# Optimization experiments

Measured on AMD Instinct MI355X. Metric: run time of the kernel, lower is better.

## Reference

```python
import jax, jax.numpy as jnp
import numpy as np

N_TOTAL = 200000
DIM = 256
N_GRAPHS = 8192
N_ITERS = 6


def setup_inputs() -> dict:
    key = jax.random.key(0)
    k1, k2, k3, k4, k5, k6 = jax.random.split(key, 6)
    x = jax.random.normal(k1, (N_TOTAL, DIM), dtype=jnp.float32)
    batch = jnp.sort(jax.random.randint(k2, (N_TOTAL,), 0, N_GRAPHS)).astype(jnp.int32)
    bound = 1.0 / np.sqrt(DIM)
    W_ih = jax.random.uniform(k3, (4 * DIM, DIM), jnp.float32, -bound, bound)
    W_hh = jax.random.uniform(k4, (4 * DIM, DIM), jnp.float32, -bound, bound)
    b_ih = jax.random.uniform(k5, (4 * DIM,), jnp.float32, -bound, bound)
    b_hh = jax.random.uniform(k6, (4 * DIM,), jnp.float32, -bound, bound)
    return {"x": x, "batch": batch, "n_graphs": N_GRAPHS,
            "W_ih": W_ih, "W_hh": W_hh, "b_ih": b_ih, "b_hh": b_hh}


def _lstm_cell(inp, h, c, W_ih, W_hh, b_ih, b_hh):
    # PyTorch LSTMCell: gates ordered i, f, g, o
    gates = inp @ W_ih.T + b_ih + h @ W_hh.T + b_hh
    i, f, g, o = jnp.split(gates, 4, axis=-1)
    c_new = jax.nn.sigmoid(f) * c + jax.nn.sigmoid(i) * jnp.tanh(g)
    h_new = jax.nn.sigmoid(o) * jnp.tanh(c_new)
    return h_new, c_new


def reference(x, batch, n_graphs, W_ih, W_hh, b_ih, b_hh):
    dim = x.shape[1]
    h = jnp.zeros((n_graphs, dim), x.dtype)
    c = jnp.zeros((n_graphs, dim), x.dtype)
    readout = jnp.zeros((n_graphs, dim), x.dtype)
    for _ in range(N_ITERS):
        # attention scores per node: <x_v, q_{g(v)}>
        scores = jnp.sum(x * h[batch], axis=-1)  # (N,)
        # torch scatter_reduce_ amax with zero init includes the 0 -> max(seg_max, 0)
        seg_max = jax.ops.segment_max(scores, batch, num_segments=n_graphs,
                                      indices_are_sorted=True)
        seg_max = jnp.maximum(seg_max, 0.0)
        e = jnp.exp(scores - seg_max[batch])
        seg_sum = jax.ops.segment_sum(e, batch, num_segments=n_graphs,
                                      indices_are_sorted=True)
        w = e / (seg_sum[batch] + 1e-8)  # (N,)
        readout = jax.ops.segment_sum(x * w[:, None], batch, num_segments=n_graphs,
                                      indices_are_sorted=True)  # (G, dim)
        h, c = _lstm_cell(readout, h, c, W_ih, W_hh, b_ih, b_hh)
    return jnp.concatenate([h, readout], axis=-1)  # (G, 2*dim)
```

## Files before the change

### kernel.cpp

```cpp
#include <hip/hip_runtime.h>
#include <hip/hip_bf16.h>
#include <stdint.h>

#define DIM 256
#define NG 8192
#define KDIM 512
#define GDIM 1024
#define N_ITERS 6
#define CHUNK 32

#define BM 128
#define BN 128
#define BK 64

typedef __hip_bfloat16 bf16;
typedef __attribute__((ext_vector_type(8))) short bf16x8;
typedef __attribute__((ext_vector_type(4))) float f32x4;

__device__ __forceinline__ void async16(void* lds, const void* g) {
    __builtin_amdgcn_global_load_lds((const __attribute__((address_space(1))) void*)g,
                                     (__attribute__((address_space(3))) void*)lds, 16, 0, 0);
}

__device__ __forceinline__ float fast_sigmoid(float v) {
    return 1.0f / (1.0f + __expf(-v));
}
__device__ __forceinline__ float fast_tanh(float v) {
    float e = __expf(2.0f * v);
    return (e - 1.0f) / (e + 1.0f);
}

__global__ void k_offsets(const int* __restrict__ batch, int* __restrict__ offs, int n_nodes) {
    int v = blockIdx.x * blockDim.x + threadIdx.x;
    if (v >= n_nodes) return;
    int b = batch[v];
    int bp = (v == 0) ? -1 : batch[v - 1];
    for (int g = bp + 1; g <= b; ++g) offs[g] = v;
    if (v == n_nodes - 1) {
        for (int g = b + 1; g <= NG; ++g) offs[g] = n_nodes;
    }
}

__global__ void k_prep_w(const float* __restrict__ Wih, const float* __restrict__ Whh,
                         const float* __restrict__ bih, const float* __restrict__ bhh,
                         bf16* __restrict__ Wcat, float* __restrict__ bsum) {
    int idx = blockIdx.x * blockDim.x + threadIdx.x;
    if (idx < GDIM * KDIM) {
        int j = idx >> 9;
        int k = idx & (KDIM - 1);
        float v = (k < DIM) ? Wih[j * DIM + k] : Whh[j * DIM + (k - DIM)];
        Wcat[idx] = __float2bfloat16(v);
    }
    if (idx < GDIM) bsum[idx] = bih[idx] + bhh[idx];
}

__global__ void k_zero(float* __restrict__ h, float* __restrict__ c, bf16* __restrict__ Acat) {
    int i = blockIdx.x * blockDim.x + threadIdx.x;
    if (i < NG * DIM) { h[i] = 0.0f; c[i] = 0.0f; }
    if (i < NG * KDIM) Acat[i] = __float2bfloat16(0.0f);
}

__global__ __launch_bounds__(256) void k_att(const float* __restrict__ x,
                                             const float* __restrict__ h,
                                             const int* __restrict__ offs,
                                             float* __restrict__ readout,
                                             bf16* __restrict__ Acat) {
    const int g = blockIdx.x;
    const int tid = threadIdx.x;
    const int wave = tid >> 6, lane = tid & 63;

    __shared__ float xs[CHUNK][DIM];
    __shared__ float sc[CHUNK];
    __shared__ float esh[CHUNK];
    __shared__ float hs[DIM];

    hs[tid] = h[(size_t)g * DIM + tid];
    __syncthreads();
    const float4 hreg = *(const float4*)&hs[lane * 4];

    const int start = offs[g], end = offs[g + 1];
    float racc = 0.0f;
    float m = 0.0f;
    float s = 0.0f;

    for (int base = start; base < end; base += CHUNK) {
        const int cnt = min(CHUNK, end - base);
        for (int i = wave; i < cnt; i += 4) {
            const float4 xv = ((const float4*)(x + (size_t)(base + i) * DIM))[lane];
            ((float4*)xs[i])[lane] = xv;
            float d = xv.x * hreg.x + xv.y * hreg.y + xv.z * hreg.z + xv.w * hreg.w;
            #pragma unroll
            for (int off = 32; off > 0; off >>= 1) d += __shfl_xor(d, off);
            if (lane == 0) sc[i] = d;
        }
        __syncthreads();
        float cmax = m;
        for (int i = 0; i < cnt; ++i) cmax = fmaxf(cmax, sc[i]);
        const float alpha = __expf(m - cmax);
        racc *= alpha;
        s *= alpha;
        if (tid < cnt) esh[tid] = __expf(sc[tid] - cmax);
        m = cmax;
        __syncthreads();
        for (int i = 0; i < cnt; ++i) {
            const float e = esh[i];
            s += e;
            racc += e * xs[i][tid];
        }
        __syncthreads();
    }

    const float out = racc / (s + 1e-8f);
    readout[(size_t)g * DIM + tid] = out;
    Acat[(size_t)g * KDIM + tid] = __float2bfloat16(out);
}

__global__ __launch_bounds__(256) void k_gemm(const bf16* __restrict__ A,
                                              const bf16* __restrict__ B,
                                              const float* __restrict__ bsum,
                                              float* __restrict__ gates) {
    __shared__ bf16 As[BM * BK];
    __shared__ bf16 Bs[BN * BK];

    const int tid = threadIdx.x;
    const int wave = tid >> 6, lane = tid & 63;
    const int m0 = blockIdx.x * BM;
    const int n0 = blockIdx.y * BN;
    const int wr = wave >> 1, wc = wave & 1;

    f32x4 acc[4][4] = {};

    const int row_in_grp = lane >> 3;
    const int chunk = lane & 7;

    for (int k0 = 0; k0 < KDIM; k0 += BK) {
        #pragma unroll
        for (int i = 0; i < 4; ++i) {
            const int row = wave * 32 + i * 8 + row_in_grp;
            async16(&As[(wave * 32 + i * 8) * BK],
                    A + (size_t)(m0 + row) * KDIM + k0 + chunk * 8);
        }
        #pragma unroll
        for (int i = 0; i < 4; ++i) {
            const int row = wave * 32 + i * 8 + row_in_grp;
            async16(&Bs[(wave * 32 + i * 8) * BK],
                    B + (size_t)(n0 + row) * KDIM + k0 + chunk * 8);
        }
        asm volatile("s_waitcnt vmcnt(0)" ::: "memory");
        __syncthreads();

        #pragma unroll
        for (int ks = 0; ks < BK; ks += 32) {
            bf16x8 a[4], b[4];
            #pragma unroll
            for (int mi = 0; mi < 4; ++mi)
                a[mi] = *(const bf16x8*)&As[(wr * 64 + mi * 16 + (lane & 15)) * BK + ks + (lane >> 4) * 8];
            #pragma unroll
            for (int ni = 0; ni < 4; ++ni)
                b[ni] = *(const bf16x8*)&Bs[(wc * 64 + ni * 16 + (lane & 15)) * BK + ks + (lane >> 4) * 8];
            #pragma unroll
            for (int mi = 0; mi < 4; ++mi)
                #pragma unroll
                for (int ni = 0; ni < 4; ++ni)
                    acc[mi][ni] = __builtin_amdgcn_mfma_f32_16x16x32_bf16(a[mi], b[ni], acc[mi][ni], 0, 0, 0);
        }
        __syncthreads();
    }

    #pragma unroll
    for (int mi = 0; mi < 4; ++mi) {
        #pragma unroll
        for (int ni = 0; ni < 4; ++ni) {
            const int col = n0 + wc * 64 + ni * 16 + (lane & 15);
            const float bv = bsum[col];
            #pragma unroll
            for (int r = 0; r < 4; ++r) {
                const int row = m0 + wr * 64 + mi * 16 + (lane >> 4) * 4 + r;
                gates[(size_t)row * GDIM + col] = acc[mi][ni][r] + bv;
            }
        }
    }
}

__global__ void k_cell(const float* __restrict__ gates, float* __restrict__ c,
                       float* __restrict__ h, bf16* __restrict__ Acat) {
    int idx = blockIdx.x * blockDim.x + threadIdx.x;
    if (idx >= NG * DIM) return;
    const int g = idx >> 8, d = idx & (DIM - 1);
    const float* gr = gates + (size_t)g * GDIM;
    const float vi = gr[d];
    const float vf = gr[d + 256];
    const float vg = gr[d + 512];
    const float vo = gr[d + 768];
    const float cn = fast_sigmoid(vf) * c[idx] + fast_sigmoid(vi) * fast_tanh(vg);
    const float hn = fast_sigmoid(vo) * fast_tanh(cn);
    c[idx] = cn;
    h[idx] = hn;
    Acat[(size_t)g * KDIM + DIM + d] = __float2bfloat16(hn);
}

__global__ void k_out(const float* __restrict__ h, const float* __restrict__ readout,
                      float* __restrict__ out) {
    int idx = blockIdx.x * blockDim.x + threadIdx.x;
    if (idx >= NG * KDIM) return;
    const int g = idx >> 9, d = idx & (KDIM - 1);
    out[idx] = (d < DIM) ? h[(size_t)g * DIM + d] : readout[(size_t)g * DIM + (d - DIM)];
}

extern "C" void kernel_launch(void* const* d_in, const int* in_sizes, int n_in,
                              void* d_out, int out_size, void* d_ws, size_t ws_size,
                              hipStream_t stream) {
    const float* x     = (const float*)d_in[0];
    const int*   batch = (const int*)d_in[1];
    const float* Wih   = (const float*)d_in[3];
    const float* Whh   = (const float*)d_in[4];
    const float* bih   = (const float*)d_in[5];
    const float* bhh   = (const float*)d_in[6];
    const int n_nodes  = in_sizes[0] / DIM;
    float* out = (float*)d_out;

    char* ws = (char*)d_ws;
    size_t off = 0;
    auto alloc = [&](size_t bytes) -> void* {
        off = (off + 255) & ~(size_t)255;
        void* p = ws + off;
        off += bytes;
        return p;
    };
    int*   offs    = (int*)  alloc((size_t)(NG + 1) * sizeof(int));
    bf16*  Wcat    = (bf16*) alloc((size_t)GDIM * KDIM * sizeof(bf16));
    float* bsum    = (float*)alloc((size_t)GDIM * sizeof(float));
    bf16*  Acat    = (bf16*) alloc((size_t)NG * KDIM * sizeof(bf16));
    float* h       = (float*)alloc((size_t)NG * DIM * sizeof(float));
    float* c       = (float*)alloc((size_t)NG * DIM * sizeof(float));
    float* readout = (float*)alloc((size_t)NG * DIM * sizeof(float));
    float* gates   = (float*)alloc((size_t)NG * GDIM * sizeof(float));
    (void)ws_size; (void)n_in; (void)out_size;

    k_offsets<<<(n_nodes + 255) / 256, 256, 0, stream>>>(batch, offs, n_nodes);
    k_prep_w<<<(GDIM * KDIM + 255) / 256, 256, 0, stream>>>(Wih, Whh, bih, bhh, Wcat, bsum);
    k_zero<<<(NG * KDIM + 255) / 256, 256, 0, stream>>>(h, c, Acat);

    for (int it = 0; it < N_ITERS; ++it) {
        k_att<<<NG, 256, 0, stream>>>(x, h, offs, readout, Acat);
        k_gemm<<<dim3(NG / BM, GDIM / BN), 256, 0, stream>>>(Acat, Wcat, bsum, gates);
        k_cell<<<(NG * DIM + 255) / 256, 256, 0, stream>>>(gates, c, h, Acat);
    }
    k_out<<<(NG * KDIM + 255) / 256, 256, 0, stream>>>(h, readout, out);
}
```

Measured before the change: 838.5 us.

## Fuse LSTM cell into GEMM epilogue and cache x as fp16 after first pass

Interleaves the gate rows of the weight matrix so each GEMM tile holds all four gates for its hidden units, which lets the LSTM cell update run in the GEMM epilogue and removes the fp32 gates round trip and the separate cell kernel. The A operand is double-buffered so the fused epilogue can write the new h half without racing other tiles. The first attention pass also writes an fp16 copy of x, and later passes read that copy, halving the dominant x traffic. The risk is lower precision in the attention scores and readout from fp16 x, plus extra LDS syncs in the epilogue.

```diff
diff --git a/kernel.cpp b/kernel.cpp
--- a/kernel.cpp
+++ b/kernel.cpp
@@ -1,5 +1,6 @@
 #include <hip/hip_runtime.h>
 #include <hip/hip_bf16.h>
+#include <hip/hip_fp16.h>
 #include <stdint.h>
 
 #define DIM 256
@@ -16,18 +17,31 @@
 typedef __hip_bfloat16 bf16;
 typedef __attribute__((ext_vector_type(8))) short bf16x8;
 typedef __attribute__((ext_vector_type(4))) float f32x4;
+typedef __attribute__((ext_vector_type(8))) unsigned short u16x8;
+typedef __attribute__((ext_vector_type(4))) unsigned short u16x4;
 
 __device__ __forceinline__ void async16(void* lds, const void* g) {
     __builtin_amdgcn_global_load_lds((const __attribute__((address_space(1))) void*)g,
                                      (__attribute__((address_space(3))) void*)lds, 16, 0, 0);
 }
-
 __device__ __forceinline__ float fast_sigmoid(float v) {
     return 1.0f / (1.0f + __expf(-v));
 }
 __device__ __forceinline__ float fast_tanh(float v) {
     float e = __expf(2.0f * v);
     return (e - 1.0f) / (e + 1.0f);
+}
+__device__ __forceinline__ unsigned short f2bf(float v) {
+    __hip_bfloat16 t = __float2bfloat16(v);
+    unsigned short u; __builtin_memcpy(&u, &t, 2); return u;
+}
+__device__ __forceinline__ unsigned short f2h(float v) {
+    __half t = __float2half_rn(v);
+    unsigned short u; __builtin_memcpy(&u, &t, 2); return u;
+}
+__device__ __forceinline__ float h2f(unsigned short u) {
+    __half t; __builtin_memcpy(&t, &u, 2);
+    return __half2float(t);
 }
 
 __global__ void k_offsets(const int* __restrict__ batch, int* __restrict__ offs, int n_nodes) {
@@ -46,37 +60,50 @@
                          bf16* __restrict__ Wcat, float* __restrict__ bsum) {
     int idx = blockIdx.x * blockDim.x + threadIdx.x;
     if (idx < GDIM * KDIM) {
-        int j = idx >> 9;
+        int n = idx >> 9;
         int k = idx & (KDIM - 1);
+        int d = n >> 2, gate = n & 3;
+        int j = gate * DIM + d;
         float v = (k < DIM) ? Wih[j * DIM + k] : Whh[j * DIM + (k - DIM)];
         Wcat[idx] = __float2bfloat16(v);
     }
-    if (idx < GDIM) bsum[idx] = bih[idx] + bhh[idx];
-}
-
-__global__ void k_zero(float* __restrict__ h, float* __restrict__ c, bf16* __restrict__ Acat) {
+    if (idx < GDIM) {
+        int d = idx >> 2, gate = idx & 3;
+        int j = gate * DIM + d;
+        bsum[idx] = bih[j] + bhh[j];
+    }
+}
+
+__global__ void k_zero(float* __restrict__ h, float* __restrict__ c, bf16* __restrict__ Acat0) {
     int i = blockIdx.x * blockDim.x + threadIdx.x;
-    if (i < NG * DIM) { h[i] = 0.0f; c[i] = 0.0f; }
-    if (i < NG * KDIM) Acat[i] = __float2bfloat16(0.0f);
-}
-
-__global__ __launch_bounds__(256) void k_att(const float* __restrict__ x,
+    if (i >= NG * DIM) return;
+    h[i] = 0.0f; c[i] = 0.0f;
+    Acat0[(size_t)(i >> 8) * KDIM + DIM + (i & 255)] = __float2bfloat16(0.0f);
+}
+
+template <bool FIRST>
+__global__ __launch_bounds__(256) void k_att(const float* __restrict__ xf,
+                                             unsigned short* __restrict__ xb,
                                              const float* __restrict__ h,
                                              const int* __restrict__ offs,
                                              float* __restrict__ readout,
-                                             bf16* __restrict__ Acat) {
+                                             bf16* __restrict__ AcatOut) {
     const int g = blockIdx.x;
     const int tid = threadIdx.x;
     const int wave = tid >> 6, lane = tid & 63;
-
-    __shared__ float xs[CHUNK][DIM];
+    const int sub = lane >> 5, hl = lane & 31;
+
+    __shared__ unsigned short xs[CHUNK][DIM];
     __shared__ float sc[CHUNK];
     __shared__ float esh[CHUNK];
-    __shared__ float hs[DIM];
-
-    hs[tid] = h[(size_t)g * DIM + tid];
-    __syncthreads();
-    const float4 hreg = *(const float4*)&hs[lane * 4];
+
+    float hreg[8];
+    {
+        const float4 h0 = *(const float4*)&h[(size_t)g * DIM + hl * 8];
+        const float4 h1 = *(const float4*)&h[(size_t)g * DIM + hl * 8 + 4];
+        hreg[0] = h0.x; hreg[1] = h0.y; hreg[2] = h0.z; hreg[3] = h0.w;
+        hreg[4] = h1.x; hreg[5] = h1.y; hreg[6] = h1.z; hreg[7] = h1.w;
+    }
 
     const int start = offs[g], end = offs[g + 1];
     float racc = 0.0f;
@@ -85,13 +112,28 @@
 
     for (int base = start; base < end; base += CHUNK) {
         const int cnt = min(CHUNK, end - base);
-        for (int i = wave; i < cnt; i += 4) {
-            const float4 xv = ((const float4*)(x + (size_t)(base + i) * DIM))[lane];
-            ((float4*)xs[i])[lane] = xv;
-            float d = xv.x * hreg.x + xv.y * hreg.y + xv.z * hreg.z + xv.w * hreg.w;
-            #pragma unroll
-            for (int off = 32; off > 0; off >>= 1) d += __shfl_xor(d, off);
-            if (lane == 0) sc[i] = d;
+        for (int i = wave * 2; i < cnt; i += 8) {
+            const int r = i + sub;
+            if (r < cnt) {
+                u16x8 pk;
+                float dt = 0.0f;
+                if (FIRST) {
+                    const float4 a = *(const float4*)&xf[(size_t)(base + r) * DIM + hl * 8];
+                    const float4 b = *(const float4*)&xf[(size_t)(base + r) * DIM + hl * 8 + 4];
+                    float xv[8] = {a.x, a.y, a.z, a.w, b.x, b.y, b.z, b.w};
+                    #pragma unroll
+                    for (int j = 0; j < 8; ++j) { pk[j] = f2h(xv[j]); dt = fmaf(xv[j], hreg[j], dt); }
+                    *(u16x8*)&xb[(size_t)(base + r) * DIM + hl * 8] = pk;
+                } else {
+                    pk = *(const u16x8*)&xb[(size_t)(base + r) * DIM + hl * 8];
+                    #pragma unroll
+                    for (int j = 0; j < 8; ++j) dt = fmaf(h2f(pk[j]), hreg[j], dt);
+                }
+                *(u16x8*)&xs[r][hl * 8] = pk;
+                #pragma unroll
+                for (int off = 16; off > 0; off >>= 1) dt += __shfl_xor(dt, off);
+                if (hl == 0) sc[r] = dt;
+            }
         }
         __syncthreads();
         float cmax = m;
@@ -105,22 +147,26 @@
         for (int i = 0; i < cnt; ++i) {
             const float e = esh[i];
             s += e;
-            racc += e * xs[i][tid];
+            racc = fmaf(e, h2f(xs[i][tid]), racc);
         }
         __syncthreads();
     }
 
     const float out = racc / (s + 1e-8f);
     readout[(size_t)g * DIM + tid] = out;
-    Acat[(size_t)g * KDIM + tid] = __float2bfloat16(out);
-}
-
-__global__ __launch_bounds__(256) void k_gemm(const bf16* __restrict__ A,
-                                              const bf16* __restrict__ B,
-                                              const float* __restrict__ bsum,
-                                              float* __restrict__ gates) {
-    __shared__ bf16 As[BM * BK];
-    __shared__ bf16 Bs[BN * BK];
+    AcatOut[(size_t)g * KDIM + tid] = __float2bfloat16(out);
+}
+
+__global__ __launch_bounds__(256) void k_gemm_cell(const bf16* __restrict__ A,
+                                                   const bf16* __restrict__ W,
+                                                   const float* __restrict__ bsum,
+                                                   float* __restrict__ cst,
+                                                   float* __restrict__ hst,
+                                                   bf16* __restrict__ AcatN) {
+    __shared__ union {
+        struct { bf16 As[BM * BK]; bf16 Bs[BN * BK]; } st;
+        float ep[32][132];
+    } sm;
 
     const int tid = threadIdx.x;
     const int wave = tid >> 6, lane = tid & 63;
@@ -130,21 +176,20 @@
 
     f32x4 acc[4][4] = {};
 
-    const int row_in_grp = lane >> 3;
     const int chunk = lane & 7;
 
     for (int k0 = 0; k0 < KDIM; k0 += BK) {
         #pragma unroll
         for (int i = 0; i < 4; ++i) {
-            const int row = wave * 32 + i * 8 + row_in_grp;
-            async16(&As[(wave * 32 + i * 8) * BK],
-                    A + (size_t)(m0 + row) * KDIM + k0 + chunk * 8);
+            const int grp = wave * 32 + i * 8;
+            async16(&sm.st.As[grp * BK],
+                    A + (size_t)(m0 + grp + (lane >> 3)) * KDIM + k0 + chunk * 8);
         }
         #pragma unroll
         for (int i = 0; i < 4; ++i) {
-            const int row = wave * 32 + i * 8 + row_in_grp;
-            async16(&Bs[(wave * 32 + i * 8) * BK],
-                    B + (size_t)(n0 + row) * KDIM + k0 + chunk * 8);
+            const int grp = wave * 32 + i * 8;
+            async16(&sm.st.Bs[grp * BK],
+                    W + (size_t)(n0 + grp + (lane >> 3)) * KDIM + k0 + chunk * 8);
         }
         asm volatile("s_waitcnt vmcnt(0)" ::: "memory");
         __syncthreads();
@@ -154,10 +199,10 @@
             bf16x8 a[4], b[4];
             #pragma unroll
             for (int mi = 0; mi < 4; ++mi)
-                a[mi] = *(const bf16x8*)&As[(wr * 64 + mi * 16 + (lane & 15)) * BK + ks + (lane >> 4) * 8];
+                a[mi] = *(const bf16x8*)&sm.st.As[(wr * 64 + mi * 16 + (lane & 15)) * BK + ks + (lane >> 4) * 8];
             #pragma unroll
             for (int ni = 0; ni < 4; ++ni)
-                b[ni] = *(const bf16x8*)&Bs[(wc * 64 + ni * 16 + (lane & 15)) * BK + ks + (lane >> 4) * 8];
+                b[ni] = *(const bf16x8*)&sm.st.Bs[(wc * 64 + ni * 16 + (lane & 15)) * BK + ks + (lane >> 4) * 8];
             #pragma unroll
             for (int mi = 0; mi < 4; ++mi)
                 #pragma unroll
@@ -167,36 +212,44 @@
         __syncthreads();
     }
 
+    float bv[4];
+    #pragma unroll
+    for (int ni = 0; ni < 4; ++ni)
+        bv[ni] = bsum[n0 + wc * 64 + ni * 16 + (lane & 15)];
+
+    const int d0 = n0 >> 2;
+    const int lr = tid >> 3;
+    const int dd = (tid & 7) * 4;
+
     #pragma unroll
     for (int mi = 0; mi < 4; ++mi) {
+        __syncthreads();
         #pragma unroll
         for (int ni = 0; ni < 4; ++ni) {
-            const int col = n0 + wc * 64 + ni * 16 + (lane & 15);
-            const float bv = bsum[col];
+            const int colL = wc * 64 + ni * 16 + (lane & 15);
             #pragma unroll
             for (int r = 0; r < 4; ++r) {
-                const int row = m0 + wr * 64 + mi * 16 + (lane >> 4) * 4 + r;
-                gates[(size_t)row * GDIM + col] = acc[mi][ni][r] + bv;
+                const int lrow = wr * 16 + (lane >> 4) * 4 + r;
+                sm.ep[lrow][colL] = acc[mi][ni][r] + bv[ni];
             }
         }
-    }
-}
-
-__global__ void k_cell(const float* __restrict__ gates, float* __restrict__ c,
-                       float* __restrict__ h, bf16* __restrict__ Acat) {
-    int idx = blockIdx.x * blockDim.x + threadIdx.x;
-    if (idx >= NG * DIM) return;
-    const int g = idx >> 8, d = idx & (DIM - 1);
-    const float* gr = gates + (size_t)g * GDIM;
-    const float vi = gr[d];
-    const float vf = gr[d + 256];
-    const float vg = gr[d + 512];
-    const float vo = gr[d + 768];
-    const float cn = fast_sigmoid(vf) * c[idx] + fast_sigmoid(vi) * fast_tanh(vg);
-    const float hn = fast_sigmoid(vo) * fast_tanh(cn);
-    c[idx] = cn;
-    h[idx] = hn;
-    Acat[(size_t)g * KDIM + DIM + d] = __float2bfloat16(hn);
+        __syncthreads();
+        const int grow = m0 + (lr >> 4) * 64 + mi * 16 + (lr & 15);
+        const int d = d0 + dd;
+        float co[4], cn[4], hn[4];
+        *(float4*)co = *(const float4*)&cst[(size_t)grow * DIM + d];
+        u16x4 hb;
+        #pragma unroll
+        for (int j = 0; j < 4; ++j) {
+            const float4 q = *(const float4*)&sm.ep[lr][(dd + j) * 4];
+            cn[j] = fast_sigmoid(q.y) * co[j] + fast_sigmoid(q.x) * fast_tanh(q.z);
+            hn[j] = fast_sigmoid(q.w) * fast_tanh(cn[j]);
+            hb[j] = f2bf(hn[j]);
+        }
+        *(float4*)&cst[(size_t)grow * DIM + d] = *(float4*)cn;
+        *(float4*)&hst[(size_t)grow * DIM + d] = *(float4*)hn;
+        *(u16x4*)&AcatN[(size_t)grow * KDIM + DIM + d] = hb;
+    }
 }
 
 __global__ void k_out(const float* __restrict__ h, const float* __restrict__ readout,
@@ -230,21 +283,26 @@
     int*   offs    = (int*)  alloc((size_t)(NG + 1) * sizeof(int));
     bf16*  Wcat    = (bf16*) alloc((size_t)GDIM * KDIM * sizeof(bf16));
     float* bsum    = (float*)alloc((size_t)GDIM * sizeof(float));
-    bf16*  Acat    = (bf16*) alloc((size_t)NG * KDIM * sizeof(bf16));
+    bf16*  Acat0   = (bf16*) alloc((size_t)NG * KDIM * sizeof(bf16));
+    bf16*  Acat1   = (bf16*) alloc((size_t)NG * KDIM * sizeof(bf16));
     float* h       = (float*)alloc((size_t)NG * DIM * sizeof(float));
     float* c       = (float*)alloc((size_t)NG * DIM * sizeof(float));
     float* readout = (float*)alloc((size_t)NG * DIM * sizeof(float));
-    float* gates   = (float*)alloc((size_t)NG * GDIM * sizeof(float));
+    unsigned short* xb = (unsigned short*)alloc((size_t)n_nodes * DIM * sizeof(unsigned short));
     (void)ws_size; (void)n_in; (void)out_size;
 
     k_offsets<<<(n_nodes + 255) / 256, 256, 0, stream>>>(batch, offs, n_nodes);
     k_prep_w<<<(GDIM * KDIM + 255) / 256, 256, 0, stream>>>(Wih, Whh, bih, bhh, Wcat, bsum);
-    k_zero<<<(NG * KDIM + 255) / 256, 256, 0, stream>>>(h, c, Acat);
+    k_zero<<<(NG * DIM + 255) / 256, 256, 0, stream>>>(h, c, Acat0);
 
     for (int it = 0; it < N_ITERS; ++it) {
-        k_att<<<NG, 256, 0, stream>>>(x, h, offs, readout, Acat);
-        k_gemm<<<dim3(NG / BM, GDIM / BN), 256, 0, stream>>>(Acat, Wcat, bsum, gates);
-        k_cell<<<(NG * DIM + 255) / 256, 256, 0, stream>>>(gates, c, h, Acat);
+        bf16* Ain  = (it & 1) ? Acat1 : Acat0;
+        bf16* Aout = (it & 1) ? Acat0 : Acat1;
+        if (it == 0)
+            k_att<true><<<NG, 256, 0, stream>>>(x, xb, h, offs, readout, Ain);
+        else
+            k_att<false><<<NG, 256, 0, stream>>>(x, xb, h, offs, readout, Ain);
+        k_gemm_cell<<<dim3(NG / BM, GDIM / BN), 256, 0, stream>>>(Ain, Wcat, bsum, c, h, Aout);
     }
     k_out<<<(NG * KDIM + 255) / 256, 256, 0, stream>>>(h, readout, out);
 }
```

Result: slower. 883.9 us (+5.4%).
